# Kernel optimization log

Measured on AMD Instinct MI355X. Metric: run time of the kernel, lower is better.

The kernel has to match this reference:

```python
import jax, jax.numpy as jnp
import numpy as np


def setup_inputs() -> dict:
    key = jax.random.key(0)
    k1, k2 = jax.random.split(key)
    B, H, W = 64, 512, 512
    return {
        "output": jax.random.normal(k1, (B, H, W), dtype=jnp.float32),
        "target": jax.random.normal(k2, (B, H, W), dtype=jnp.float32),
        "patch_size": 8,
    }


def reference(output, target, patch_size):
    B, H, W = output.shape
    p = patch_size
    nh, nw = H // p, W // p  # torch.unfold drops any remainder
    def patches(x):
        # [B,H,W] -> [B, nh*nw, p*p], row-major over (i, j) like the nested loop
        x = x[:, : nh * p, : nw * p]
        x = x.reshape(B, nh, p, nw, p).transpose(0, 1, 3, 2, 4)
        return x.reshape(B, nh * nw, p * p)
    op = patches(output)
    tp = patches(target)
    # per-patch L1 loss (mean reduction) and per-patch mean of target
    losses = jnp.mean(jnp.abs(op - tp), axis=-1)  # [B, nh*nw]
    means = jnp.mean(tp, axis=-1)                 # [B, nh*nw]
    agree = jnp.argmax(losses, axis=-1) == jnp.argmax(means, axis=-1)  # [B]
    num_true = jnp.sum(agree).astype(jnp.int32)
    total_num = jnp.int32(B)
    num_false = total_num - num_true
    correctness = num_true.astype(jnp.float32) / total_num.astype(jnp.float32)
    return (total_num, num_true, num_false, correctness)
```

## Files before the change

kernel.cpp:

```cpp
#include <hip/hip_runtime.h>


__device__ __forceinline__ unsigned ordf(float f) {
    unsigned u = __float_as_uint(f);
    return u ^ ((u >> 31) ? 0xFFFFFFFFu : 0x80000000u);
}

__device__ __forceinline__ unsigned long long umax64(unsigned long long a,
                                                     unsigned long long b) {
    return a > b ? a : b;
}

__device__ __forceinline__ void loadc(float4 (&O)[8], float4 (&G)[8],
                                      const float* po, const float* pt) {
#pragma unroll
    for (int r = 0; r < 8; ++r)
        O[r] = *reinterpret_cast<const float4*>(po + (size_t)r * 512);
#pragma unroll
    for (int r = 0; r < 8; ++r)
        G[r] = *reinterpret_cast<const float4*>(pt + (size_t)r * 512);
}

__device__ __forceinline__ void consume(const float4 (&O)[8], const float4 (&G)[8],
                                        int ws_, int l, int k,
                                        unsigned long long& kl,
                                        unsigned long long& km) {
    float sA = 0.f, sT = 0.f;
#pragma unroll
    for (int r = 0; r < 8; ++r) {
        sA += fabsf(O[r].x - G[r].x) + fabsf(O[r].y - G[r].y)
            + fabsf(O[r].z - G[r].z) + fabsf(O[r].w - G[r].w);
        sT += G[r].x + G[r].y + G[r].z + G[r].w;
    }
    sA += __shfl_xor(sA, 1);
    sT += __shfl_xor(sT, 1);
    const int tb  = ws_ + 32 * k;
    const int idx = (tb >> 1) * 64 + (tb & 1) * 32 + (l >> 1);
    kl = umax64(kl, ((unsigned long long)ordf(sA) << 32) | (unsigned)(4095 - idx));
    km = umax64(km, ((unsigned long long)ordf(sT) << 32) | (unsigned)(4095 - idx));
}

__global__ __launch_bounds__(256, 2)
void patch_kernel(const float* __restrict__ outp,
                  const float* __restrict__ tgt,
                  unsigned long long* __restrict__ wsL,
                  unsigned long long* __restrict__ wsM) {
    const int t   = threadIdx.x;
    const int g   = blockIdx.x * 4 + (t >> 6);
    const int l   = t & 63;
    const int b   = g >> 5;
    const int ws_ = g & 31;

    const size_t base0 = (size_t)b * 262144 + (size_t)(ws_ >> 1) * 4096
                       + (size_t)(ws_ & 1) * 256 + (size_t)l * 4;
    const float* po = outp + base0;
    const float* pt = tgt  + base0;

    float4 oA[8], gA[8], oB[8], gB[8];
    unsigned long long kl = 0, km = 0;

    loadc(oA, gA, po,          pt);
    loadc(oB, gB, po + 65536,  pt + 65536);
    consume(oA, gA, ws_, l, 0, kl, km);
    loadc(oA, gA, po + 131072, pt + 131072);
    consume(oB, gB, ws_, l, 1, kl, km);
    loadc(oB, gB, po + 196608, pt + 196608);
    consume(oA, gA, ws_, l, 2, kl, km);
    consume(oB, gB, ws_, l, 3, kl, km);

#pragma unroll
    for (int s = 32; s > 1; s >>= 1) {
        kl = umax64(kl, __shfl_xor(kl, s));
        km = umax64(km, __shfl_xor(km, s));
    }

    if (l == 0) { wsL[g] = kl; wsM[g] = km; }
}

__global__ void finalize_kernel(const unsigned long long* __restrict__ wsL,
                                const unsigned long long* __restrict__ wsM,
                                float* __restrict__ outp) {
    const int t    = threadIdx.x;
    const int q    = t >> 2;
    const int part = t & 3;

    unsigned long long ml = 0, mm = 0;
    const int base = q * 32 + part * 8;
#pragma unroll
    for (int i = 0; i < 8; ++i) {
        ml = umax64(ml, wsL[base + i]);
        mm = umax64(mm, wsM[base + i]);
    }
    ml = umax64(ml, __shfl_xor(ml, 1));
    ml = umax64(ml, __shfl_xor(ml, 2));
    mm = umax64(mm, __shfl_xor(mm, 1));
    mm = umax64(mm, __shfl_xor(mm, 2));

    __shared__ int flags[64];
    if (part == 0)
        flags[q] = ((unsigned)ml == (unsigned)mm) ? 1 : 0;
    __syncthreads();

    if (t < 64) {
        int v = flags[t];
#pragma unroll
        for (int s = 32; s > 0; s >>= 1) v += __shfl_down(v, s);
        if (t == 0) {
            const float nt = (float)v;
            outp[0] = 64.0f;
            outp[1] = nt;
            outp[2] = 64.0f - nt;
            outp[3] = nt / 64.0f;
        }
    }
}

extern "C" void kernel_launch(void* const* d_in, const int* in_sizes, int n_in,
                              void* d_out, int out_size, void* d_ws, size_t ws_size,
                              hipStream_t stream) {
    const float* outp = (const float*)d_in[0];
    const float* tgt  = (const float*)d_in[1];

    unsigned long long* wsL = (unsigned long long*)d_ws;
    unsigned long long* wsM = wsL + 2048;

    patch_kernel<<<512, 256, 0, stream>>>(outp, tgt, wsL, wsM);
    finalize_kernel<<<1, 256, 0, stream>>>(wsL, wsM, (float*)d_out);
}
```

Measured before the change: 26.96 us.

## Stream patch tiles through LDS with async global_load_lds double buffering

Replaces direct register float4 loads with asynchronous global-to-LDS DMA (global_load_lds) into per-wave double buffers, using explicit vmcnt waits to keep two tiles in flight. Each wave now processes eight tiles instead of four, with 1024 waves in 128-thread blocks. The aim is deeper memory-level parallelism without register pressure. It adds 64KB of shared memory per block, which limits occupancy, plus an extra LDS read pass and hand-written waitcnt sequencing that is fragile.

```diff
diff --git a/kernel.cpp b/kernel.cpp
--- a/kernel.cpp
+++ b/kernel.cpp
@@ -1,93 +1,111 @@
 #include <hip/hip_runtime.h>
 
+
+typedef unsigned long long u64;
 
 __device__ __forceinline__ unsigned ordf(float f) {
     unsigned u = __float_as_uint(f);
     return u ^ ((u >> 31) ? 0xFFFFFFFFu : 0x80000000u);
 }
 
-__device__ __forceinline__ unsigned long long umax64(unsigned long long a,
-                                                     unsigned long long b) {
-    return a > b ? a : b;
+__device__ __forceinline__ u64 umax64(u64 a, u64 b) { return a > b ? a : b; }
+
+#define GLDS(gp, lp)                                                      \
+    __builtin_amdgcn_global_load_lds(                                     \
+        (const __attribute__((address_space(1))) void*)(gp),              \
+        (__attribute__((address_space(3))) void*)(lp), 16, 0, 0)
+
+__device__ __forceinline__ void dma_tile(const float* po, const float* pt,
+                                         float* buf) {
+#pragma unroll
+    for (int r = 0; r < 8; ++r)
+        GLDS(po + (size_t)r * 512, buf + r * 256);
+#pragma unroll
+    for (int r = 0; r < 8; ++r)
+        GLDS(pt + (size_t)r * 512, buf + 2048 + r * 256);
 }
 
-__device__ __forceinline__ void loadc(float4 (&O)[8], float4 (&G)[8],
-                                      const float* po, const float* pt) {
-#pragma unroll
-    for (int r = 0; r < 8; ++r)
-        O[r] = *reinterpret_cast<const float4*>(po + (size_t)r * 512);
-#pragma unroll
-    for (int r = 0; r < 8; ++r)
-        G[r] = *reinterpret_cast<const float4*>(pt + (size_t)r * 512);
-}
-
-__device__ __forceinline__ void consume(const float4 (&O)[8], const float4 (&G)[8],
-                                        int ws_, int l, int k,
-                                        unsigned long long& kl,
-                                        unsigned long long& km) {
+__device__ __forceinline__ void consume_lds(const float* buf, int l, int idx,
+                                            u64& kl, u64& km) {
+    const float4* f4 = (const float4*)buf;
     float sA = 0.f, sT = 0.f;
 #pragma unroll
     for (int r = 0; r < 8; ++r) {
-        sA += fabsf(O[r].x - G[r].x) + fabsf(O[r].y - G[r].y)
-            + fabsf(O[r].z - G[r].z) + fabsf(O[r].w - G[r].w);
-        sT += G[r].x + G[r].y + G[r].z + G[r].w;
+        const float4 o = f4[r * 64 + l];
+        const float4 g = f4[512 + r * 64 + l];
+        sA += fabsf(o.x - g.x) + fabsf(o.y - g.y)
+            + fabsf(o.z - g.z) + fabsf(o.w - g.w);
+        sT += g.x + g.y + g.z + g.w;
     }
     sA += __shfl_xor(sA, 1);
     sT += __shfl_xor(sT, 1);
-    const int tb  = ws_ + 32 * k;
-    const int idx = (tb >> 1) * 64 + (tb & 1) * 32 + (l >> 1);
-    kl = umax64(kl, ((unsigned long long)ordf(sA) << 32) | (unsigned)(4095 - idx));
-    km = umax64(km, ((unsigned long long)ordf(sT) << 32) | (unsigned)(4095 - idx));
+    kl = umax64(kl, ((u64)ordf(sA) << 32) | (unsigned)(4095 - idx));
+    km = umax64(km, ((u64)ordf(sT) << 32) | (unsigned)(4095 - idx));
 }
 
-__global__ __launch_bounds__(256, 2)
+__global__ __launch_bounds__(128)
 void patch_kernel(const float* __restrict__ outp,
                   const float* __restrict__ tgt,
-                  unsigned long long* __restrict__ wsL,
-                  unsigned long long* __restrict__ wsM) {
+                  u64* __restrict__ wsL, u64* __restrict__ wsM) {
+    __shared__ float smem[16384];
+
     const int t   = threadIdx.x;
-    const int g   = blockIdx.x * 4 + (t >> 6);
+    const int w01 = t >> 6;
     const int l   = t & 63;
-    const int b   = g >> 5;
-    const int ws_ = g & 31;
+    const int g   = blockIdx.x * 2 + w01;
+    const int b   = g >> 4;
+    const int s   = g & 15;
 
-    const size_t base0 = (size_t)b * 262144 + (size_t)(ws_ >> 1) * 4096
-                       + (size_t)(ws_ & 1) * 256 + (size_t)l * 4;
+    float* buf0 = smem + w01 * 8192;
+    float* buf1 = buf0 + 4096;
+
+    const size_t base0 = (size_t)b * 262144 + (size_t)(s >> 1) * 4096
+                       + (size_t)(s & 1) * 256 + (size_t)l * 4;
     const float* po = outp + base0;
     const float* pt = tgt  + base0;
+    const int idx0  = (s >> 1) * 64 + (s & 1) * 32 + (l >> 1);
 
-    float4 oA[8], gA[8], oB[8], gB[8];
-    unsigned long long kl = 0, km = 0;
+    u64 kl = 0, km = 0;
 
-    loadc(oA, gA, po,          pt);
-    loadc(oB, gB, po + 65536,  pt + 65536);
-    consume(oA, gA, ws_, l, 0, kl, km);
-    loadc(oA, gA, po + 131072, pt + 131072);
-    consume(oB, gB, ws_, l, 1, kl, km);
-    loadc(oB, gB, po + 196608, pt + 196608);
-    consume(oA, gA, ws_, l, 2, kl, km);
-    consume(oB, gB, ws_, l, 3, kl, km);
+    dma_tile(po, pt, buf0);
+    dma_tile(po + 32768, pt + 32768, buf1);
 
 #pragma unroll
-    for (int s = 32; s > 1; s >>= 1) {
-        kl = umax64(kl, __shfl_xor(kl, s));
-        km = umax64(km, __shfl_xor(km, s));
+    for (int k = 0; k < 8; ++k) {
+        if (k < 7) asm volatile("s_waitcnt vmcnt(16)" ::: "memory");
+        else       asm volatile("s_waitcnt vmcnt(0)"  ::: "memory");
+        __builtin_amdgcn_sched_barrier(0);
+
+        float* cb = (k & 1) ? buf1 : buf0;
+        consume_lds(cb, l, idx0 + 512 * k, kl, km);
+
+        if (k < 6) {
+            asm volatile("s_waitcnt lgkmcnt(0)" ::: "memory");
+            __builtin_amdgcn_sched_barrier(0);
+            dma_tile(po + (size_t)(k + 2) * 32768,
+                     pt + (size_t)(k + 2) * 32768, cb);
+        }
     }
 
+#pragma unroll
+    for (int sh = 32; sh > 1; sh >>= 1) {
+        kl = umax64(kl, __shfl_xor(kl, sh));
+        km = umax64(km, __shfl_xor(km, sh));
+    }
     if (l == 0) { wsL[g] = kl; wsM[g] = km; }
 }
 
-__global__ void finalize_kernel(const unsigned long long* __restrict__ wsL,
-                                const unsigned long long* __restrict__ wsM,
+__global__ void finalize_kernel(const u64* __restrict__ wsL,
+                                const u64* __restrict__ wsM,
                                 float* __restrict__ outp) {
     const int t    = threadIdx.x;
     const int q    = t >> 2;
     const int part = t & 3;
 
-    unsigned long long ml = 0, mm = 0;
-    const int base = q * 32 + part * 8;
+    u64 ml = 0, mm = 0;
+    const int base = q * 16 + part * 4;
 #pragma unroll
-    for (int i = 0; i < 8; ++i) {
+    for (int i = 0; i < 4; ++i) {
         ml = umax64(ml, wsL[base + i]);
         mm = umax64(mm, wsM[base + i]);
     }
@@ -104,7 +122,7 @@
     if (t < 64) {
         int v = flags[t];
 #pragma unroll
-        for (int s = 32; s > 0; s >>= 1) v += __shfl_down(v, s);
+        for (int sh = 32; sh > 0; sh >>= 1) v += __shfl_down(v, sh);
         if (t == 0) {
             const float nt = (float)v;
             outp[0] = 64.0f;
@@ -121,9 +139,9 @@
     const float* outp = (const float*)d_in[0];
     const float* tgt  = (const float*)d_in[1];
 
-    unsigned long long* wsL = (unsigned long long*)d_ws;
-    unsigned long long* wsM = wsL + 2048;
+    u64* wsL = (u64*)d_ws;
+    u64* wsM = wsL + 1024;
 
-    patch_kernel<<<512, 256, 0, stream>>>(outp, tgt, wsL, wsM);
+    patch_kernel<<<512, 128, 0, stream>>>(outp, tgt, wsL, wsM);
     finalize_kernel<<<1, 256, 0, stream>>>(wsL, wsM, (float*)d_out);
 }
```

After: 27.92 us. +3.6%, slower.
